# Performance work log

Hardware: AMD Instinct MI355X
Metric: run time of the kernel (lower is better)

Reference implementation:

```python
import jax, jax.numpy as jnp
import numpy as np

B, T = 2, 2048
N_EMBED = 2048
N_HEAD = 16
N_KV_HEAD = 4
HEAD_DIM = N_EMBED // N_HEAD  # 128
KV_DIM = HEAD_DIM * N_KV_HEAD  # 512
REPEAT = N_HEAD // N_KV_HEAD  # 4
THETA = 10000.0


def _apply_rope(x):
    # x: (B, T, H, D), interleaved-pair rotation as in RotaryEmbedding
    D = x.shape[-1]
    inv_freq = 1.0 / (THETA ** (jnp.arange(0, D, 2, dtype=jnp.float32) / D))  # (D/2,)
    t = jnp.arange(x.shape[1], dtype=jnp.float32)
    freqs = t[:, None] * inv_freq[None, :]            # (T, D/2)
    cos = jnp.cos(freqs)[None, :, None, :]            # (1, T, 1, D/2)
    sin = jnp.sin(freqs)[None, :, None, :]
    x1 = x[..., ::2]
    x2 = x[..., 1::2]
    even = x1 * cos - x2 * sin
    odd = x1 * sin + x2 * cos
    out = jnp.stack([even, odd], axis=-1)             # (B, T, H, D/2, 2)
    return out.reshape(x.shape)


def setup_inputs() -> dict:
    key = jax.random.key(0)
    ks = jax.random.split(key, 9)
    s_in = 1.0 / np.sqrt(N_EMBED)
    return {
        "x": jax.random.normal(ks[0], (B, T, N_EMBED), dtype=jnp.float32),
        "Wq": jax.random.normal(ks[1], (N_EMBED, N_EMBED), dtype=jnp.float32) * s_in,
        "bq": jax.random.normal(ks[2], (N_EMBED,), dtype=jnp.float32) * 0.01,
        "Wk": jax.random.normal(ks[3], (KV_DIM, N_EMBED), dtype=jnp.float32) * s_in,
        "bk": jax.random.normal(ks[4], (KV_DIM,), dtype=jnp.float32) * 0.01,
        "Wv": jax.random.normal(ks[5], (KV_DIM, N_EMBED), dtype=jnp.float32) * s_in,
        "bv": jax.random.normal(ks[6], (KV_DIM,), dtype=jnp.float32) * 0.01,
        "Wo": jax.random.normal(ks[7], (N_EMBED, N_EMBED), dtype=jnp.float32) * s_in,
        "bo": jax.random.normal(ks[8], (N_EMBED,), dtype=jnp.float32) * 0.01,
    }


def reference(x, Wq, bq, Wk, bk, Wv, bv, Wo, bo):
    Bb, Tt, _ = x.shape
    q = (x @ Wq.T + bq).reshape(Bb, Tt, N_HEAD, HEAD_DIM)
    k = (x @ Wk.T + bk).reshape(Bb, Tt, N_KV_HEAD, HEAD_DIM)
    v = (x @ Wv.T + bv).reshape(Bb, Tt, N_KV_HEAD, HEAD_DIM)
    xq = _apply_rope(q).transpose(0, 2, 1, 3)          # (B, H, T, D)
    xk = _apply_rope(k).transpose(0, 2, 1, 3)          # (B, Hkv, T, D)
    xv = v.transpose(0, 2, 1, 3)
    if REPEAT > 1:
        xk = jnp.repeat(xk, REPEAT, axis=1)            # (B, H, T, D)
        xv = jnp.repeat(xv, REPEAT, axis=1)
    qk = jnp.einsum('bhqd,bhkd->bhqk', xq, xk)         # NOTE: no pre-softmax scale (faithful)
    causal = jnp.tril(jnp.ones((Tt, Tt), dtype=bool))
    qk = jnp.where(causal[None, None, :, :], qk, -jnp.inf)
    attn = jax.nn.softmax(qk, axis=-1) * (N_EMBED ** -0.5)  # post-softmax scale, faithful to source
    o = jnp.einsum('bhqk,bhkd->bhqd', attn, xv)
    o = o.transpose(0, 2, 1, 3).reshape(Bb, Tt, N_EMBED)
    return o @ Wo.T + bo
```

## Files before the change

kernel.cpp:

```cpp
#include <hip/hip_runtime.h>
#include <math.h>


typedef __bf16 bf16;
typedef __bf16 bf16x8 __attribute__((ext_vector_type(8)));
typedef __bf16 bf16x4 __attribute__((ext_vector_type(4)));
typedef __bf16 bf16x2 __attribute__((ext_vector_type(2)));
typedef float  f32x4  __attribute__((ext_vector_type(4)));

#define T_SEQ 2048
#define NE    2048
#define NH    16
#define NKVH  4
#define HD    128
#define KVD   512
#define OSCALE 0.022097086912079608f

__device__ __forceinline__ void gload16(const void* g, void* l) {
  __builtin_amdgcn_global_load_lds(
      (const __attribute__((address_space(1))) void*)g,
      (__attribute__((address_space(3))) void*)l, 16, 0, 0);
}

__global__ __launch_bounds__(256) void prep_convert(
    const float* __restrict__ x,  const float* __restrict__ wq,
    const float* __restrict__ wk, const float* __restrict__ wv,
    const float* __restrict__ wo,
    bf16* __restrict__ xb,  bf16* __restrict__ wqb, bf16* __restrict__ wkb,
    bf16* __restrict__ wvb, bf16* __restrict__ wob)
{
  const size_t total4 = (size_t)(8388608 + 4194304 + 1048576 + 1048576 + 4194304) / 4;
  for (size_t i = (size_t)blockIdx.x * blockDim.x + threadIdx.x; i < total4;
       i += (size_t)gridDim.x * blockDim.x) {
    size_t e = i * 4;
    const float* s; bf16* d; size_t off;
    if      (e <  8388608u) { s = x;  d = xb;  off = e; }
    else if (e < 12582912u) { s = wq; d = wqb; off = e -  8388608u; }
    else if (e < 13631488u) { s = wk; d = wkb; off = e - 12582912u; }
    else if (e < 14680064u) { s = wv; d = wvb; off = e - 13631488u; }
    else                    { s = wo; d = wob; off = e - 14680064u; }
    float4 v = *(const float4*)(s + off);
    bf16x4 o = {(bf16)v.x, (bf16)v.y, (bf16)v.z, (bf16)v.w};
    *(bf16x4*)(d + off) = o;
  }
}

__global__ __launch_bounds__(256) void rope_init(float2* __restrict__ rope)
{
  int i = blockIdx.x * 256 + threadIdx.x;
  int t = i >> 6, p = i & 63;
  float invf = powf(10000.f, -(float)p * (1.f / 64.f));
  double frd = (double)((float)t * invf);
  rope[i] = make_float2((float)cos(frd), (float)sin(frd));
}

__device__ __forceinline__ void mfma_gemm_128(
    const bf16* __restrict__ Ag,
    const bf16* __restrict__ Bg,
    f32x4 acc[4][4])
{
  __shared__ bf16 As[128][32];
  __shared__ bf16 Bs[128][32];
  const int tid  = threadIdx.x;
  const int wave = tid >> 6, lane = tid & 63;
  const int g = lane >> 4, c = lane & 15;
  const int wm = wave >> 1, wn = wave & 1;

  const f32x4 zf = {0.f, 0.f, 0.f, 0.f};
  #pragma unroll
  for (int mi = 0; mi < 4; ++mi)
    #pragma unroll
    for (int ni = 0; ni < 4; ++ni) acc[mi][ni] = zf;

  const int lr = lane >> 2;
  const int lc = (lane & 3) * 8;
  const bf16* aG0 = Ag + (size_t)(wave * 16 + lr) * NE + lc;
  const bf16* aG1 = aG0 + (size_t)64 * NE;
  const bf16* bG0 = Bg + (size_t)(wave * 16 + lr) * NE + lc;
  const bf16* bG1 = bG0 + (size_t)64 * NE;
  bf16* aL0 = &As[wave * 16][0];
  bf16* aL1 = &As[64 + wave * 16][0];
  bf16* bL0 = &Bs[wave * 16][0];
  bf16* bL1 = &Bs[64 + wave * 16][0];

  for (int k0 = 0; k0 < NE; k0 += 32) {
    __syncthreads();
    gload16(aG0 + k0, aL0);
    gload16(aG1 + k0, aL1);
    gload16(bG0 + k0, bL0);
    gload16(bG1 + k0, bL1);
    __syncthreads();
    bf16x8 af[4], bfr[4];
    #pragma unroll
    for (int mi = 0; mi < 4; ++mi)
      af[mi] = *(const bf16x8*)&As[wm * 64 + mi * 16 + c][g * 8];
    #pragma unroll
    for (int ni = 0; ni < 4; ++ni)
      bfr[ni] = *(const bf16x8*)&Bs[wn * 64 + ni * 16 + c][g * 8];
    #pragma unroll
    for (int mi = 0; mi < 4; ++mi)
      #pragma unroll
      for (int ni = 0; ni < 4; ++ni)
        acc[mi][ni] = __builtin_amdgcn_mfma_f32_16x16x32_bf16(
            af[mi], bfr[ni], acc[mi][ni], 0, 0, 0);
  }
}

__device__ __forceinline__ int xcd_swz(int bid, int nwg) {
  return (bid & 7) * (nwg >> 3) + (bid >> 3);
}

__global__ __launch_bounds__(256) void qkv_mfma(
    const bf16* __restrict__ xb,  const bf16* __restrict__ wqb,
    const bf16* __restrict__ wkb, const bf16* __restrict__ wvb,
    const float* __restrict__ bq, const float* __restrict__ bk,
    const float* __restrict__ bv, const float2* __restrict__ rope,
    bf16* __restrict__ q_ws, bf16* __restrict__ k_ws, bf16* __restrict__ vT_ws)
{
  const int wid = xcd_swz(blockIdx.x, 768);
  const int n0 = (wid % 24) * 128;
  const int m0 = (wid / 24) * 128;
  int region; const bf16* Wp; const float* bp; int nl0;
  if (n0 < NE)            { region = 0; Wp = wqb; bp = bq; nl0 = n0; }
  else if (n0 < NE + KVD) { region = 1; Wp = wkb; bp = bk; nl0 = n0 - NE; }
  else                    { region = 2; Wp = wvb; bp = bv; nl0 = n0 - NE - KVD; }

  f32x4 acc[4][4];
  mfma_gemm_128(xb + (size_t)m0 * NE, Wp + (size_t)nl0 * NE, acc);

  const int tid = threadIdx.x, wave = tid >> 6, lane = tid & 63;
  const int g = lane >> 4, c = lane & 15;
  const int wm = wave >> 1, wn = wave & 1;
  const int bbase = m0 >> 11;
  const int t0base = (m0 & (T_SEQ - 1)) + wm * 64;

  if (region < 2) {
    bf16* dst = (region == 0) ? q_ws : k_ws;
    const int nheads_stride = (region == 0) ? NH : NKVH;
    #pragma unroll
    for (int ni = 0; ni < 4; ++ni) {
      const int nloc = nl0 + wn * 64 + ni * 16 + c;
      const float bias = bp[nloc];
      const int d  = nloc & (HD - 1);
      const int p  = d >> 1;
      const int hh = nloc >> 7;
      const size_t base = ((size_t)bbase * nheads_stride + hh) * (size_t)T_SEQ * HD;
      #pragma unroll
      for (int mi = 0; mi < 4; ++mi) {
        #pragma unroll
        for (int r = 0; r < 4; ++r) {
          const int t = t0base + mi * 16 + g * 4 + r;
          float val = acc[mi][ni][r] + bias;
          float other = __shfl_xor(val, 1);
          float2 cs = rope[t * 64 + p];
          float res = (c & 1) ? fmaf(other, cs.y, val * cs.x)
                              : fmaf(val, cs.x, -(other * cs.y));
          float rpair = __shfl_xor(res, 1);
          if (!(c & 1)) {
            bf16x2 pk = {(bf16)res, (bf16)rpair};
            *(bf16x2*)&dst[base + (size_t)t * HD + d] = pk;
          }
        }
      }
    }
  } else {
    #pragma unroll
    for (int ni = 0; ni < 4; ++ni) {
      const int nloc = nl0 + wn * 64 + ni * 16 + c;
      const float bias = bp[nloc];
      const int d  = nloc & (HD - 1);
      const int hh = nloc >> 7;
      const size_t vrow = ((size_t)bbase * NKVH + hh) * HD + d;
      #pragma unroll
      for (int mi = 0; mi < 4; ++mi) {
        const int t0 = t0base + mi * 16 + g * 4;
        bf16x4 pk = {(bf16)(acc[mi][ni][0] + bias), (bf16)(acc[mi][ni][1] + bias),
                     (bf16)(acc[mi][ni][2] + bias), (bf16)(acc[mi][ni][3] + bias)};
        *(bf16x4*)&vT_ws[vrow * T_SEQ + t0] = pk;
      }
    }
  }
}

__global__ __launch_bounds__(256, 4) void attn_mfma(
    const bf16* __restrict__ q_ws, const bf16* __restrict__ k_ws,
    const bf16* __restrict__ vT_ws, bf16* __restrict__ o_ws)
{
  __shared__ __align__(16) char smem[40960];
  char* Ks = smem;
  char* Vs = smem + 16384;
  char* Ps = smem + 32768;

  const int tid = threadIdx.x, wave = tid >> 6, lane = tid & 63;
  const int g = lane >> 4, c = lane & 15;
  const int bid = blockIdx.x;
  const int u = bid & 31, v = bid >> 5;
  const int h = u & 15, b = u >> 4;
  const int qt = (v < 16) ? v : (47 - v);
  const int kvh = h >> 2;

  const bf16* Qg = q_ws + (((size_t)b * NH + h) * T_SEQ + qt * 64 + wave * 16) * HD;
  const bf16* Kg = k_ws + ((size_t)b * NKVH + kvh) * (size_t)T_SEQ * HD;
  const bf16* Vg = vT_ws + ((size_t)b * NKVH + kvh) * (size_t)HD * T_SEQ;

  bf16x8 qf[4];
  #pragma unroll
  for (int kc = 0; kc < 4; ++kc)
    qf[kc] = *(const bf16x8*)(Qg + (size_t)c * HD + kc * 32 + g * 8);

  const f32x4 zf = {0.f, 0.f, 0.f, 0.f};
  f32x4 o_acc[8];
  #pragma unroll
  for (int i = 0; i < 8; ++i) o_acc[i] = zf;

  float m_run[4], l_part[4];
  #pragma unroll
  for (int r = 0; r < 4; ++r) { m_run[r] = -1e30f; l_part[r] = 0.f; }

  const int qrow_base = qt * 64 + wave * 16 + g * 4;
  const int ks_row = tid >> 4;
  const int ks_cb  = (tid & 15) * 16;
  const int vs_row = tid >> 3;
  const int vs_cb  = (tid & 7) * 16;
  const int swzc   = (c & 7) << 4;
  const int nkt = qt + 1;

  bf16x8 kreg[4], vreg[4];
  #pragma unroll
  for (int i = 0; i < 4; ++i) {
    int row = ks_row + i * 16;
    kreg[i] = *(const bf16x8*)(Kg + (size_t)row * HD + (ks_cb >> 1));
  }
  #pragma unroll
  for (int i = 0; i < 4; ++i) {
    int d = vs_row + i * 32;
    vreg[i] = *(const bf16x8*)(Vg + (size_t)d * T_SEQ + (vs_cb >> 1));
  }

  for (int kt = 0; kt < nkt; ++kt) {
    const int kb0 = kt * 64;
    __syncthreads();
    #pragma unroll
    for (int i = 0; i < 4; ++i) {
      int row = ks_row + i * 16;
      *(bf16x8*)(Ks + row * 256 + (ks_cb ^ ((row & 7) << 4))) = kreg[i];
    }
    #pragma unroll
    for (int i = 0; i < 4; ++i) {
      int d = vs_row + i * 32;
      *(bf16x8*)(Vs + d * 128 + (vs_cb ^ ((d & 7) << 4))) = vreg[i];
    }
    __syncthreads();

    if (kt + 1 < nkt) {
      const int nb0 = kb0 + 64;
      #pragma unroll
      for (int i = 0; i < 4; ++i) {
        int row = ks_row + i * 16;
        kreg[i] = *(const bf16x8*)(Kg + (size_t)(nb0 + row) * HD + (ks_cb >> 1));
      }
      #pragma unroll
      for (int i = 0; i < 4; ++i) {
        int d = vs_row + i * 32;
        vreg[i] = *(const bf16x8*)(Vg + (size_t)d * T_SEQ + nb0 + (vs_cb >> 1));
      }
    }

    f32x4 s[4];
    #pragma unroll
    for (int cf = 0; cf < 4; ++cf) s[cf] = zf;
    __builtin_amdgcn_s_setprio(1);
    #pragma unroll
    for (int cf = 0; cf < 4; ++cf)
      #pragma unroll
      for (int kc = 0; kc < 4; ++kc) {
        bf16x8 kf = *(const bf16x8*)(Ks + (cf * 16 + c) * 256 +
                                     ((kc * 64 + g * 16) ^ swzc));
        s[cf] = __builtin_amdgcn_mfma_f32_16x16x32_bf16(qf[kc], kf, s[cf], 0, 0, 0);
      }
    __builtin_amdgcn_s_setprio(0);

    if (kt == qt) {
      #pragma unroll
      for (int cf = 0; cf < 4; ++cf) {
        int key = kb0 + cf * 16 + c;
        #pragma unroll
        for (int r = 0; r < 4; ++r)
          if (key > qrow_base + r) s[cf][r] = -1e30f;
      }
    }

    float pmax[4];
    #pragma unroll
    for (int r = 0; r < 4; ++r) {
      float m2 = fmaxf(fmaxf(s[0][r], s[1][r]), fmaxf(s[2][r], s[3][r]));
      m2 = fmaxf(m2, __shfl_xor(m2, 1));
      m2 = fmaxf(m2, __shfl_xor(m2, 2));
      m2 = fmaxf(m2, __shfl_xor(m2, 4));
      m2 = fmaxf(m2, __shfl_xor(m2, 8));
      pmax[r] = m2;
    }
    int ok = (pmax[0] <= m_run[0] + 8.f) & (pmax[1] <= m_run[1] + 8.f) &
             (pmax[2] <= m_run[2] + 8.f) & (pmax[3] <= m_run[3] + 8.f);
    if (!__all(ok)) {
      #pragma unroll
      for (int r = 0; r < 4; ++r) {
        float mn = fmaxf(m_run[r], pmax[r]);
        float corr = __expf(m_run[r] - mn);
        m_run[r] = mn;
        l_part[r] *= corr;
        #pragma unroll
        for (int d0 = 0; d0 < 8; ++d0) o_acc[d0][r] *= corr;
      }
    }
    #pragma unroll
    for (int cf = 0; cf < 4; ++cf)
      #pragma unroll
      for (int r = 0; r < 4; ++r) {
        float p = __expf(s[cf][r] - m_run[r]);
        s[cf][r] = p;
        l_part[r] += p;
      }

    char* Pw = Ps + wave * 2048;
    #pragma unroll
    for (int cf = 0; cf < 4; ++cf)
      #pragma unroll
      for (int r = 0; r < 4; ++r) {
        int row = g * 4 + r;
        *(bf16*)(Pw + row * 128 + (((cf * 16 + c) * 2) ^ ((row & 7) << 4))) =
            (bf16)s[cf][r];
      }

    bf16x8 pa0 = *(const bf16x8*)(Pw + c * 128 + ((g * 16) ^ swzc));
    bf16x8 pa1 = *(const bf16x8*)(Pw + c * 128 + ((64 + g * 16) ^ swzc));
    __builtin_amdgcn_s_setprio(1);
    #pragma unroll
    for (int d0 = 0; d0 < 8; ++d0) {
      bf16x8 v0 = *(const bf16x8*)(Vs + (d0 * 16 + c) * 128 + ((g * 16) ^ swzc));
      bf16x8 v1 = *(const bf16x8*)(Vs + (d0 * 16 + c) * 128 + ((64 + g * 16) ^ swzc));
      o_acc[d0] = __builtin_amdgcn_mfma_f32_16x16x32_bf16(pa0, v0, o_acc[d0], 0, 0, 0);
      o_acc[d0] = __builtin_amdgcn_mfma_f32_16x16x32_bf16(pa1, v1, o_acc[d0], 0, 0, 0);
    }
    __builtin_amdgcn_s_setprio(0);
  }

  float f[4];
  #pragma unroll
  for (int r = 0; r < 4; ++r) {
    float lt = l_part[r];
    lt += __shfl_xor(lt, 1); lt += __shfl_xor(lt, 2);
    lt += __shfl_xor(lt, 4); lt += __shfl_xor(lt, 8);
    f[r] = OSCALE / lt;
  }
  #pragma unroll
  for (int d0 = 0; d0 < 8; ++d0)
    #pragma unroll
    for (int r = 0; r < 4; ++r) {
      float val = o_acc[d0][r] * f[r];
      float pv = __shfl_xor(val, 1);
      if (!(c & 1)) {
        bf16x2 pk = {(bf16)val, (bf16)pv};
        size_t row = (size_t)b * T_SEQ + qt * 64 + wave * 16 + g * 4 + r;
        int col = h * HD + d0 * 16 + c;
        *(bf16x2*)&o_ws[row * NE + col] = pk;
      }
    }
}

__global__ __launch_bounds__(256) void out_proj_mfma(
    const bf16* __restrict__ ob, const bf16* __restrict__ wob,
    const float* __restrict__ bo, float* __restrict__ out)
{
  const int wid = xcd_swz(blockIdx.x, 512);
  const int n0 = (wid % 16) * 128;
  const int m0 = (wid / 16) * 128;
  f32x4 acc[4][4];
  mfma_gemm_128(ob + (size_t)m0 * NE, wob + (size_t)n0 * NE, acc);

  const int tid = threadIdx.x, wave = tid >> 6, lane = tid & 63;
  const int g = lane >> 4, c = lane & 15;
  const int wm = wave >> 1, wn = wave & 1;
  #pragma unroll
  for (int ni = 0; ni < 4; ++ni) {
    const int n = n0 + wn * 64 + ni * 16 + c;
    const float bias = bo[n];
    #pragma unroll
    for (int mi = 0; mi < 4; ++mi)
      #pragma unroll
      for (int r = 0; r < 4; ++r) {
        const int m = m0 + wm * 64 + mi * 16 + g * 4 + r;
        out[(size_t)m * NE + n] = acc[mi][ni][r] + bias;
      }
  }
}

extern "C" void kernel_launch(void* const* d_in, const int* in_sizes, int n_in,
                              void* d_out, int out_size, void* d_ws, size_t ws_size,
                              hipStream_t stream)
{
  const float* x  = (const float*)d_in[0];
  const float* Wq = (const float*)d_in[1];
  const float* bq = (const float*)d_in[2];
  const float* Wk = (const float*)d_in[3];
  const float* bk = (const float*)d_in[4];
  const float* Wv = (const float*)d_in[5];
  const float* bv = (const float*)d_in[6];
  const float* Wo = (const float*)d_in[7];
  const float* bo = (const float*)d_in[8];
  float* out = (float*)d_out;

  bf16* xb    = (bf16*)d_ws;
  bf16* wqb   = xb    + 8388608;
  bf16* wkb   = wqb   + 4194304;
  bf16* wvb   = wkb   + 1048576;
  bf16* wob   = wvb   + 1048576;
  bf16* q_ws  = wob   + 4194304;
  bf16* k_ws  = q_ws  + 8388608;
  bf16* vT_ws = k_ws  + 2097152;
  bf16* o_ws  = vT_ws + 2097152;
  float2* rope = (float2*)(o_ws + 8388608);

  prep_convert<<<2048, 256, 0, stream>>>(x, Wq, Wk, Wv, Wo, xb, wqb, wkb, wvb, wob);
  rope_init<<<512, 256, 0, stream>>>(rope);
  qkv_mfma<<<768, 256, 0, stream>>>(xb, wqb, wkb, wvb, bq, bk, bv, rope,
                                    q_ws, k_ws, vT_ws);
  attn_mfma<<<1024, 256, 0, stream>>>(q_ws, k_ws, vT_ws, o_ws);
  out_proj_mfma<<<512, 256, 0, stream>>>(o_ws, wob, bo, out);
}
```

Baseline: 441.0 us.

## Double-buffer GEMM LDS tiles and simplify attention K/V prefetch registers

The shared GEMM helper now uses two LDS buffers, so the global-to-LDS load of the next 32-wide K slice is issued before the MFMAs on the current slice. This halves the barriers per slice and overlaps load latency with compute, at the cost of double the LDS footprint, which may reduce occupancy. In the attention kernel the K/V prefetch is rewritten with scalar register variables and precomputed swizzle offsets. The prefetch is also made unconditional by reloading the current tile on the last iteration, which removes a branch but adds redundant loads.

```diff
diff --git a/kernel.cpp b/kernel.cpp
--- a/kernel.cpp
+++ b/kernel.cpp
@@ -59,8 +59,8 @@
     const bf16* __restrict__ Bg,
     f32x4 acc[4][4])
 {
-  __shared__ bf16 As[128][32];
-  __shared__ bf16 Bs[128][32];
+  __shared__ bf16 As[2][128][32];
+  __shared__ bf16 Bs[2][128][32];
   const int tid  = threadIdx.x;
   const int wave = tid >> 6, lane = tid & 63;
   const int g = lane >> 4, c = lane & 15;
@@ -78,32 +78,42 @@
   const bf16* aG1 = aG0 + (size_t)64 * NE;
   const bf16* bG0 = Bg + (size_t)(wave * 16 + lr) * NE + lc;
   const bf16* bG1 = bG0 + (size_t)64 * NE;
-  bf16* aL0 = &As[wave * 16][0];
-  bf16* aL1 = &As[64 + wave * 16][0];
-  bf16* bL0 = &Bs[wave * 16][0];
-  bf16* bL1 = &Bs[64 + wave * 16][0];
-
-  for (int k0 = 0; k0 < NE; k0 += 32) {
+
+#define G_STAGE(B, K) do {                                    \
+    gload16(aG0 + (K), &As[B][wave * 16][0]);                 \
+    gload16(aG1 + (K), &As[B][64 + wave * 16][0]);            \
+    gload16(bG0 + (K), &Bs[B][wave * 16][0]);                 \
+    gload16(bG1 + (K), &Bs[B][64 + wave * 16][0]);            \
+  } while (0)
+
+#define G_COMPUTE(B) do {                                     \
+    bf16x8 af[4], bfr[4];                                     \
+    _Pragma("unroll")                                         \
+    for (int mi = 0; mi < 4; ++mi)                            \
+      af[mi] = *(const bf16x8*)&As[B][wm * 64 + mi * 16 + c][g * 8]; \
+    _Pragma("unroll")                                         \
+    for (int ni = 0; ni < 4; ++ni)                            \
+      bfr[ni] = *(const bf16x8*)&Bs[B][wn * 64 + ni * 16 + c][g * 8]; \
+    _Pragma("unroll")                                         \
+    for (int mi = 0; mi < 4; ++mi)                            \
+      _Pragma("unroll")                                       \
+      for (int ni = 0; ni < 4; ++ni)                          \
+        acc[mi][ni] = __builtin_amdgcn_mfma_f32_16x16x32_bf16(\
+            af[mi], bfr[ni], acc[mi][ni], 0, 0, 0);           \
+  } while (0)
+
+  G_STAGE(0, 0);
+  __syncthreads();
+  for (int k0 = 0; k0 < NE; k0 += 64) {
+    G_STAGE(1, k0 + 32);
+    G_COMPUTE(0);
     __syncthreads();
-    gload16(aG0 + k0, aL0);
-    gload16(aG1 + k0, aL1);
-    gload16(bG0 + k0, bL0);
-    gload16(bG1 + k0, bL1);
+    if (k0 + 64 < NE) G_STAGE(0, k0 + 64);
+    G_COMPUTE(1);
     __syncthreads();
-    bf16x8 af[4], bfr[4];
-    #pragma unroll
-    for (int mi = 0; mi < 4; ++mi)
-      af[mi] = *(const bf16x8*)&As[wm * 64 + mi * 16 + c][g * 8];
-    #pragma unroll
-    for (int ni = 0; ni < 4; ++ni)
-      bfr[ni] = *(const bf16x8*)&Bs[wn * 64 + ni * 16 + c][g * 8];
-    #pragma unroll
-    for (int mi = 0; mi < 4; ++mi)
-      #pragma unroll
-      for (int ni = 0; ni < 4; ++ni)
-        acc[mi][ni] = __builtin_amdgcn_mfma_f32_16x16x32_bf16(
-            af[mi], bfr[ni], acc[mi][ni], 0, 0, 0);
-  }
+  }
+#undef G_STAGE
+#undef G_COMPUTE
 }
 
 __device__ __forceinline__ int xcd_swz(int bid, int nwg) {
@@ -223,48 +233,43 @@
   const int vs_row = tid >> 3;
   const int vs_cb  = (tid & 7) * 16;
   const int swzc   = (c & 7) << 4;
+  const int swz_k  = ks_cb ^ ((ks_row & 7) << 4);
+  const int swz_v  = vs_cb ^ ((vs_row & 7) << 4);
+  const int ks_ce  = ks_cb >> 1;
+  const int vs_ce  = vs_cb >> 1;
   const int nkt = qt + 1;
 
-  bf16x8 kreg[4], vreg[4];
-  #pragma unroll
-  for (int i = 0; i < 4; ++i) {
-    int row = ks_row + i * 16;
-    kreg[i] = *(const bf16x8*)(Kg + (size_t)row * HD + (ks_cb >> 1));
-  }
-  #pragma unroll
-  for (int i = 0; i < 4; ++i) {
-    int d = vs_row + i * 32;
-    vreg[i] = *(const bf16x8*)(Vg + (size_t)d * T_SEQ + (vs_cb >> 1));
-  }
+  bf16x8 k0r = *(const bf16x8*)(Kg + (size_t)(ks_row     ) * HD + ks_ce);
+  bf16x8 k1r = *(const bf16x8*)(Kg + (size_t)(ks_row + 16) * HD + ks_ce);
+  bf16x8 k2r = *(const bf16x8*)(Kg + (size_t)(ks_row + 32) * HD + ks_ce);
+  bf16x8 k3r = *(const bf16x8*)(Kg + (size_t)(ks_row + 48) * HD + ks_ce);
+  bf16x8 v0r = *(const bf16x8*)(Vg + (size_t)(vs_row     ) * T_SEQ + vs_ce);
+  bf16x8 v1r = *(const bf16x8*)(Vg + (size_t)(vs_row + 32) * T_SEQ + vs_ce);
+  bf16x8 v2r = *(const bf16x8*)(Vg + (size_t)(vs_row + 64) * T_SEQ + vs_ce);
+  bf16x8 v3r = *(const bf16x8*)(Vg + (size_t)(vs_row + 96) * T_SEQ + vs_ce);
 
   for (int kt = 0; kt < nkt; ++kt) {
     const int kb0 = kt * 64;
     __syncthreads();
-    #pragma unroll
-    for (int i = 0; i < 4; ++i) {
-      int row = ks_row + i * 16;
-      *(bf16x8*)(Ks + row * 256 + (ks_cb ^ ((row & 7) << 4))) = kreg[i];
-    }
-    #pragma unroll
-    for (int i = 0; i < 4; ++i) {
-      int d = vs_row + i * 32;
-      *(bf16x8*)(Vs + d * 128 + (vs_cb ^ ((d & 7) << 4))) = vreg[i];
-    }
+    *(bf16x8*)(Ks + (ks_row     ) * 256 + swz_k) = k0r;
+    *(bf16x8*)(Ks + (ks_row + 16) * 256 + swz_k) = k1r;
+    *(bf16x8*)(Ks + (ks_row + 32) * 256 + swz_k) = k2r;
+    *(bf16x8*)(Ks + (ks_row + 48) * 256 + swz_k) = k3r;
+    *(bf16x8*)(Vs + (vs_row     ) * 128 + swz_v) = v0r;
+    *(bf16x8*)(Vs + (vs_row + 32) * 128 + swz_v) = v1r;
+    *(bf16x8*)(Vs + (vs_row + 64) * 128 + swz_v) = v2r;
+    *(bf16x8*)(Vs + (vs_row + 96) * 128 + swz_v) = v3r;
     __syncthreads();
 
-    if (kt + 1 < nkt) {
-      const int nb0 = kb0 + 64;
-      #pragma unroll
-      for (int i = 0; i < 4; ++i) {
-        int row = ks_row + i * 16;
-        kreg[i] = *(const bf16x8*)(Kg + (size_t)(nb0 + row) * HD + (ks_cb >> 1));
-      }
-      #pragma unroll
-      for (int i = 0; i < 4; ++i) {
-        int d = vs_row + i * 32;
-        vreg[i] = *(const bf16x8*)(Vg + (size_t)d * T_SEQ + nb0 + (vs_cb >> 1));
-      }
-    }
+    const int nb0 = (kt + 1 < nkt) ? (kb0 + 64) : kb0;
+    k0r = *(const bf16x8*)(Kg + (size_t)(nb0 + ks_row     ) * HD + ks_ce);
+    k1r = *(const bf16x8*)(Kg + (size_t)(nb0 + ks_row + 16) * HD + ks_ce);
+    k2r = *(const bf16x8*)(Kg + (size_t)(nb0 + ks_row + 32) * HD + ks_ce);
+    k3r = *(const bf16x8*)(Kg + (size_t)(nb0 + ks_row + 48) * HD + ks_ce);
+    v0r = *(const bf16x8*)(Vg + (size_t)(vs_row     ) * T_SEQ + nb0 + vs_ce);
+    v1r = *(const bf16x8*)(Vg + (size_t)(vs_row + 32) * T_SEQ + nb0 + vs_ce);
+    v2r = *(const bf16x8*)(Vg + (size_t)(vs_row + 64) * T_SEQ + nb0 + vs_ce);
+    v3r = *(const bf16x8*)(Vg + (size_t)(vs_row + 96) * T_SEQ + nb0 + vs_ce);
 
     f32x4 s[4];
     #pragma unroll
```

Result: slower. 520.3 us (+18.0%).
